# Performance work log

Measured on AMD Instinct MI355X. Metric: run time of the kernel, lower is better.

## Reference

```python
import jax, jax.numpy as jnp
import numpy as np

N_NODES = 50000
N_EDGES = 640000
D = 128      # in_feats
OUT = 128    # out_feats


def setup_inputs() -> dict:
    key = jax.random.key(0)
    ks = jax.random.split(key, 8)
    feat = jax.random.normal(ks[0], (N_NODES, D), dtype=jnp.float32)
    weight = jax.random.uniform(ks[1], (N_EDGES,), dtype=jnp.float32)
    src = jax.random.randint(ks[2], (N_EDGES,), 0, N_NODES, dtype=jnp.int64)
    dst = jax.random.randint(ks[3], (N_EDGES,), 0, N_NODES, dtype=jnp.int64)
    # xavier_uniform with relu gain ~ sqrt(2)*sqrt(6/(fan_in+fan_out))
    g = np.sqrt(2.0)
    lim_pool = g * np.sqrt(6.0 / (D + D))
    lim_neigh = g * np.sqrt(6.0 / (2 * D + OUT))
    W_pool = jax.random.uniform(ks[4], (D, D), dtype=jnp.float32, minval=-lim_pool, maxval=lim_pool)
    b_pool = jnp.zeros((D,), dtype=jnp.float32)
    W_neigh = jax.random.uniform(ks[5], (OUT, 2 * D), dtype=jnp.float32, minval=-lim_neigh, maxval=lim_neigh)
    b_neigh = jnp.zeros((OUT,), dtype=jnp.float32)
    return {"feat": feat, "weight": weight, "src": src, "dst": dst,
            "W_pool": W_pool, "b_pool": b_pool, "W_neigh": W_neigh, "b_neigh": b_neigh}


def reference(feat, weight, src, dst, W_pool, b_pool, W_neigh, b_neigh):
    n = feat.shape[0]
    # fc_pool: h = feat @ W_pool.T + b_pool  -> [N, D]
    h = feat @ W_pool.T + b_pool
    # u_mul_e: per-edge message m_e = h[src_e] * w_e  -> [E, D]
    m = h[src] * weight[:, None]
    # max reduce over incoming edges (scatter-max by dst)
    neigh = jax.ops.segment_max(m, dst, num_segments=n)
    # zero-degree nodes get 0 (segment_max fills empties with -inf)
    deg = jax.ops.segment_sum(jnp.ones_like(weight), dst, num_segments=n)
    neigh = jnp.where(deg[:, None] > 0, neigh, jnp.zeros((), dtype=feat.dtype))
    # fc_neigh on concat(feat, neigh)
    rst = jnp.concatenate([feat, neigh], axis=1) @ W_neigh.T + b_neigh
    return rst
```

## Files before the change

kernel.cpp:

```cpp
#include <hip/hip_runtime.h>
#include <cstdint>
#include <cstddef>

#define N_NODES 50000
#define N_EDGES 640000
#define DF 128

#define NBUCK 196
#define BCAP  6144
#define PA_BLOCKS 250

typedef __attribute__((ext_vector_type(8))) short bf16x8;
typedef __attribute__((ext_vector_type(4))) float f32x4;

__device__ inline unsigned short f2bf(float f) {
    unsigned int u = __float_as_uint(f);
    return (unsigned short)((u + 0x7fffu + ((u >> 16) & 1u)) >> 16);
}

#define NF4 (N_NODES * DF / 4)
#define NWG (3 * 2048)
__global__ __launch_bounds__(256) void k1_setup_bucket(
    const float* __restrict__ feat,
    const float* __restrict__ W_pool,
    const float* __restrict__ W_neigh,
    const int* __restrict__ src,
    const int* __restrict__ dst,
    const float* __restrict__ w,
    unsigned short* __restrict__ featb,
    unsigned short* __restrict__ Wp_f,
    unsigned short* __restrict__ Wn1_f,
    unsigned short* __restrict__ Wn2_f,
    int* __restrict__ bucketcnt,
    uint2* __restrict__ staging)
{
    int bid = blockIdx.x;
    int t = threadIdx.x;
    if (bid < PA_BLOCKS) {
        __shared__ int cnt[NBUCK];
        __shared__ int runbase[NBUCK];
        int base = bid * 2560;
        if (t < NBUCK) cnt[t] = 0;
        __syncthreads();
        uint2 rec[10];
        int bk[10];
        #pragma unroll
        for (int i = 0; i < 10; ++i) {
            int e = base + i * 256 + t;
            int s = src[e], d = dst[e];
            bk[i] = d >> 8;
            rec[i].x = (unsigned int)s | ((unsigned int)(d & 255) << 16);
            rec[i].y = __float_as_uint(w[e]);
            atomicAdd(&cnt[bk[i]], 1);
        }
        __syncthreads();
        if (t < NBUCK) {
            runbase[t] = atomicAdd(&bucketcnt[t], cnt[t]);
            cnt[t] = 0;
        }
        __syncthreads();
        #pragma unroll
        for (int i = 0; i < 10; ++i) {
            int r = atomicAdd(&cnt[bk[i]], 1);
            int pos = runbase[bk[i]] + r;
            if (pos < BCAP) staging[bk[i] * BCAP + pos] = rec[i];
        }
    } else if (bid < 250 + NF4 / 256) {
        int idx = (bid - PA_BLOCKS) * 256 + t;
        float4 v = ((const float4*)feat)[idx];
        ushort4 o;
        o.x = f2bf(v.x); o.y = f2bf(v.y); o.z = f2bf(v.z); o.w = f2bf(v.w);
        ((ushort4*)featb)[idx] = o;
    } else {
        int g = (bid - PA_BLOCKS - NF4 / 256) * 256 + t;
        int m = g >> 11;
        int r8 = g & 2047;
        int L = r8 & 63, tt = (r8 >> 6) & 3, c = r8 >> 8;
        int o = c * 16 + (L & 15);
        int kb = tt * 32 + (L >> 4) * 8;
        const float* srcp;
        unsigned short* dstp;
        if (m == 0)      { srcp = W_pool  + o * 128 + kb;       dstp = Wp_f;  }
        else if (m == 1) { srcp = W_neigh + o * 256 + kb;       dstp = Wn1_f; }
        else             { srcp = W_neigh + o * 256 + 128 + kb; dstp = Wn2_f; }
        ushort4 lo, hi;
        float4 a = ((const float4*)srcp)[0];
        float4 b = ((const float4*)srcp)[1];
        lo.x = f2bf(a.x); lo.y = f2bf(a.y); lo.z = f2bf(a.z); lo.w = f2bf(a.w);
        hi.x = f2bf(b.x); hi.y = f2bf(b.y); hi.z = f2bf(b.z); hi.w = f2bf(b.w);
        ((ushort4*)(dstp + r8 * 8))[0] = lo;
        ((ushort4*)(dstp + r8 * 8))[1] = hi;
    }
}

#define GEMMB 196
__global__ __launch_bounds__(1024) void k2_gemm_passb(
    const unsigned short* __restrict__ featb,
    const unsigned short* __restrict__ Wp_f,
    const float* __restrict__ b_pool,
    unsigned short* __restrict__ hb,
    const int* __restrict__ bucketcnt,
    const uint2* __restrict__ staging,
    int* __restrict__ offsets,
    uint2* __restrict__ edges)
{
    int t = threadIdx.x;
    if (blockIdx.x < GEMMB) {
        int wave = blockIdx.x * 16 + (t >> 6);
        int lane = t & 63;
        int m0 = wave * 16;
        if (m0 >= N_NODES) return;
        const int n = lane & 15, quad = lane >> 4;

        f32x4 acc[8];
        #pragma unroll
        for (int c = 0; c < 8; ++c) {
            float bv = b_pool[c * 16 + n];
            acc[c] = (f32x4){bv, bv, bv, bv};
        }
        const unsigned short* aptr = featb + (size_t)(m0 + n) * DF + quad * 8;
        #pragma unroll
        for (int tt = 0; tt < 4; ++tt) {
            bf16x8 af = *(const bf16x8*)(aptr + tt * 32);
            #pragma unroll
            for (int c = 0; c < 8; ++c) {
                bf16x8 bf = *(const bf16x8*)(Wp_f + (size_t)((c * 4 + tt) * 64 + lane) * 8);
                acc[c] = __builtin_amdgcn_mfma_f32_16x16x32_bf16(af, bf, acc[c], 0, 0, 0);
            }
        }
        #pragma unroll
        for (int c = 0; c < 8; ++c)
            #pragma unroll
            for (int r = 0; r < 4; ++r)
                hb[(size_t)(m0 + quad * 4 + r) * DF + c * 16 + n] = f2bf(acc[c][r]);
    } else {
        __shared__ int dcnt[256];
        __shared__ int sc[256];
        __shared__ int bc[256];
        int b = blockIdx.x - GEMMB;

        if (t < 256) { dcnt[t] = 0; bc[t] = (t < NBUCK) ? bucketcnt[t] : 0; sc[t] = (t < NBUCK) ? bc[t] : 0; }
        __syncthreads();
        #pragma unroll
        for (int off = 1; off < 256; off <<= 1) {
            int u = (t < 256 && t >= off) ? sc[t - off] : 0;
            __syncthreads();
            if (t < 256) sc[t] += u;
            __syncthreads();
        }
        int mybase = (b > 0) ? sc[b - 1] : 0;
        int cnt = bc[b];
        __syncthreads();

        uint2 rec[6];
        int nit = (cnt + 1023) >> 10;
        for (int i = 0; i < nit; ++i) {
            int idx = i * 1024 + t;
            if (idx < cnt) {
                rec[i] = staging[(size_t)b * BCAP + idx];
                atomicAdd(&dcnt[(rec[i].x >> 16) & 255], 1);
            }
        }
        __syncthreads();
        if (t < 256) sc[t] = dcnt[t];
        __syncthreads();
        #pragma unroll
        for (int off = 1; off < 256; off <<= 1) {
            int u = (t < 256 && t >= off) ? sc[t - off] : 0;
            __syncthreads();
            if (t < 256) sc[t] += u;
            __syncthreads();
        }
        if (t < 256) {
            int node = b * 256 + t;
            int excl = sc[t] - dcnt[t];
            if (node < N_NODES) offsets[node] = mybase + excl;
            dcnt[t] = mybase + excl;
        }
        if (b == NBUCK - 1 && t == 0) offsets[N_NODES] = mybase + cnt;
        __syncthreads();
        for (int i = 0; i < nit; ++i) {
            int idx = i * 1024 + t;
            if (idx < cnt) {
                int dl = (rec[i].x >> 16) & 255;
                int pos = atomicAdd(&dcnt[dl], 1);
                uint2 fin;
                fin.x = rec[i].x & 0xFFFFu;
                fin.y = rec[i].y;
                edges[pos] = fin;
            }
        }
    }
}

__global__ __launch_bounds__(256) void neigh_max_kernel(
    const unsigned short* __restrict__ hb, const int* __restrict__ offsets,
    const uint2* __restrict__ edges,
    unsigned short* __restrict__ neighb)
{
    int gwave = (blockIdx.x * 256 + threadIdx.x) >> 6;
    if (gwave >= N_NODES) return;
    int node = __builtin_amdgcn_readfirstlane(gwave);
    int lane = threadIdx.x & 63;
    const int half = lane >> 5;
    const int q = lane & 31;

    int beg = offsets[node], end = offsets[node + 1];
    float4 acc = make_float4(-3.4e38f, -3.4e38f, -3.4e38f, -3.4e38f);

    for (int e = beg; e < end; e += 8) {
        int i1 = min(e + 1, end - 1);
        int i2 = min(e + 2, end - 1);
        int i3 = min(e + 3, end - 1);
        int i4 = min(e + 4, end - 1);
        int i5 = min(e + 5, end - 1);
        int i6 = min(e + 6, end - 1);
        int i7 = min(e + 7, end - 1);
        uint2 e0 = edges[e],  e1 = edges[i1], e2 = edges[i2], e3 = edges[i3];
        uint2 e4 = edges[i4], e5 = edges[i5], e6 = edges[i6], e7 = edges[i7];
        uint2 mA = half ? e1 : e0;
        uint2 mB = half ? e3 : e2;
        uint2 mC = half ? e5 : e4;
        uint2 mD = half ? e7 : e6;
        float wA = __uint_as_float(mA.y);
        float wB = __uint_as_float(mB.y);
        float wC = __uint_as_float(mC.y);
        float wD = __uint_as_float(mD.y);
        uint2 pA = *(const uint2*)(hb + (size_t)mA.x * DF + q * 4);
        uint2 pB = *(const uint2*)(hb + (size_t)mB.x * DF + q * 4);
        uint2 pC = *(const uint2*)(hb + (size_t)mC.x * DF + q * 4);
        uint2 pD = *(const uint2*)(hb + (size_t)mD.x * DF + q * 4);
        acc.x = fmaxf(acc.x, __uint_as_float(pA.x << 16)          * wA);
        acc.y = fmaxf(acc.y, __uint_as_float(pA.x & 0xffff0000u)  * wA);
        acc.z = fmaxf(acc.z, __uint_as_float(pA.y << 16)          * wA);
        acc.w = fmaxf(acc.w, __uint_as_float(pA.y & 0xffff0000u)  * wA);
        acc.x = fmaxf(acc.x, __uint_as_float(pB.x << 16)          * wB);
        acc.y = fmaxf(acc.y, __uint_as_float(pB.x & 0xffff0000u)  * wB);
        acc.z = fmaxf(acc.z, __uint_as_float(pB.y << 16)          * wB);
        acc.w = fmaxf(acc.w, __uint_as_float(pB.y & 0xffff0000u)  * wB);
        acc.x = fmaxf(acc.x, __uint_as_float(pC.x << 16)          * wC);
        acc.y = fmaxf(acc.y, __uint_as_float(pC.x & 0xffff0000u)  * wC);
        acc.z = fmaxf(acc.z, __uint_as_float(pC.y << 16)          * wC);
        acc.w = fmaxf(acc.w, __uint_as_float(pC.y & 0xffff0000u)  * wC);
        acc.x = fmaxf(acc.x, __uint_as_float(pD.x << 16)          * wD);
        acc.y = fmaxf(acc.y, __uint_as_float(pD.x & 0xffff0000u)  * wD);
        acc.z = fmaxf(acc.z, __uint_as_float(pD.y << 16)          * wD);
        acc.w = fmaxf(acc.w, __uint_as_float(pD.y & 0xffff0000u)  * wD);
    }

    float4 o;
    o.x = fmaxf(acc.x, __shfl_xor(acc.x, 32));
    o.y = fmaxf(acc.y, __shfl_xor(acc.y, 32));
    o.z = fmaxf(acc.z, __shfl_xor(acc.z, 32));
    o.w = fmaxf(acc.w, __shfl_xor(acc.w, 32));
    if (beg == end) o = make_float4(0.f, 0.f, 0.f, 0.f);
    if (half == 0) {
        ushort4 ob;
        ob.x = f2bf(o.x); ob.y = f2bf(o.y); ob.z = f2bf(o.z); ob.w = f2bf(o.w);
        *(ushort4*)(neighb + (size_t)node * DF + q * 4) = ob;
    }
}

__global__ __launch_bounds__(256) void gemm_out(
    const unsigned short* __restrict__ featb,
    const unsigned short* __restrict__ neighb,
    const unsigned short* __restrict__ Wn1_f,
    const unsigned short* __restrict__ Wn2_f,
    const float* __restrict__ bias,
    float* __restrict__ out)
{
    int wave = (blockIdx.x * 256 + threadIdx.x) >> 6;
    int lane = threadIdx.x & 63;
    int m0 = wave * 16;
    if (m0 >= N_NODES) return;
    const int n = lane & 15, quad = lane >> 4;

    f32x4 acc[8];
    #pragma unroll
    for (int c = 0; c < 8; ++c) {
        float bv = bias[c * 16 + n];
        acc[c] = (f32x4){bv, bv, bv, bv};
    }

    const unsigned short* a0 = featb  + (size_t)(m0 + n) * DF + quad * 8;
    const unsigned short* a1 = neighb + (size_t)(m0 + n) * DF + quad * 8;
    #pragma unroll
    for (int t = 0; t < 4; ++t) {
        bf16x8 af = *(const bf16x8*)(a0 + t * 32);
        #pragma unroll
        for (int c = 0; c < 8; ++c) {
            bf16x8 bf = *(const bf16x8*)(Wn1_f + (size_t)((c * 4 + t) * 64 + lane) * 8);
            acc[c] = __builtin_amdgcn_mfma_f32_16x16x32_bf16(af, bf, acc[c], 0, 0, 0);
        }
    }
    #pragma unroll
    for (int t = 0; t < 4; ++t) {
        bf16x8 af = *(const bf16x8*)(a1 + t * 32);
        #pragma unroll
        for (int c = 0; c < 8; ++c) {
            bf16x8 bf = *(const bf16x8*)(Wn2_f + (size_t)((c * 4 + t) * 64 + lane) * 8);
            acc[c] = __builtin_amdgcn_mfma_f32_16x16x32_bf16(af, bf, acc[c], 0, 0, 0);
        }
    }

    #pragma unroll
    for (int c = 0; c < 8; ++c)
        #pragma unroll
        for (int r = 0; r < 4; ++r)
            out[(size_t)(m0 + quad * 4 + r) * DF + c * 16 + n] = acc[c][r];
}

extern "C" void kernel_launch(void* const* d_in, const int* in_sizes, int n_in,
                              void* d_out, int out_size, void* d_ws, size_t ws_size,
                              hipStream_t stream) {
    const float* feat    = (const float*)d_in[0];
    const float* weight  = (const float*)d_in[1];
    const int*   src     = (const int*)d_in[2];
    const int*   dst     = (const int*)d_in[3];
    const float* W_pool  = (const float*)d_in[4];
    const float* b_pool  = (const float*)d_in[5];
    const float* W_neigh = (const float*)d_in[6];
    const float* b_neigh = (const float*)d_in[7];
    float* out = (float*)d_out;

    char* ws = (char*)d_ws;
    unsigned short* featb  = (unsigned short*)(ws);
    unsigned short* hb     = (unsigned short*)(ws + 12800000);
    unsigned short* neighb = (unsigned short*)(ws + 25600000);
    unsigned short* Wp_f   = (unsigned short*)(ws + 38400000);
    unsigned short* Wn1_f  = (unsigned short*)(ws + 38432768);
    unsigned short* Wn2_f  = (unsigned short*)(ws + 38465536);
    int*   offsets   = (int*)  (ws + 38498304);
    int*   bucketcnt = (int*)  (ws + 38698368);
    uint2* staging   = (uint2*)(ws + 38699392);
    uint2* edges     = (uint2*)(ws + 48333184);

    hipMemsetAsync(bucketcnt, 0, 1024, stream);

    const int K1_BLOCKS = PA_BLOCKS + NF4 / 256 + NWG / 256;
    k1_setup_bucket<<<K1_BLOCKS, 256, 0, stream>>>(
        feat, W_pool, W_neigh, src, dst, weight,
        featb, Wp_f, Wn1_f, Wn2_f, bucketcnt, staging);

    k2_gemm_passb<<<GEMMB + NBUCK, 1024, 0, stream>>>(
        featb, Wp_f, b_pool, hb, bucketcnt, staging, offsets, edges);

    neigh_max_kernel<<<(N_NODES + 3) / 4, 256, 0, stream>>>(hb, offsets, edges, neighb);

    gemm_out<<<782, 256, 0, stream>>>(
        featb, neighb, Wn1_f, Wn2_f, b_neigh, out);
}
```

Baseline: 163.1 us.

## Fuse neighbor max aggregation with output GEMM via shared-memory tile

Merges the segment-max gather kernel and the output MFMA GEMM into one kernel. Each 256-thread block reduces 16 destination nodes into an LDS tile, then its four waves each compute two 16-column output chunks from that tile plus featb. This removes the neighb round-trip through global memory and one kernel launch. In exchange, each wave processes four nodes serially, and the block barrier makes waves wait on the highest-degree node in the tile, which may reduce latency hiding in the gather.

```diff
diff --git a/kernel.cpp b/kernel.cpp
--- a/kernel.cpp
+++ b/kernel.cpp
@@ -9,6 +9,7 @@
 #define NBUCK 196
 #define BCAP  6144
 #define PA_BLOCKS 250
+#define LPAD 136
 
 typedef __attribute__((ext_vector_type(8))) short bf16x8;
 typedef __attribute__((ext_vector_type(4))) float f32x4;
@@ -193,121 +194,116 @@
     }
 }
 
-__global__ __launch_bounds__(256) void neigh_max_kernel(
-    const unsigned short* __restrict__ hb, const int* __restrict__ offsets,
+__global__ __launch_bounds__(256) void neigh_out(
+    const unsigned short* __restrict__ featb,
+    const unsigned short* __restrict__ hb,
+    const int* __restrict__ offsets,
     const uint2* __restrict__ edges,
-    unsigned short* __restrict__ neighb)
-{
-    int gwave = (blockIdx.x * 256 + threadIdx.x) >> 6;
-    if (gwave >= N_NODES) return;
-    int node = __builtin_amdgcn_readfirstlane(gwave);
-    int lane = threadIdx.x & 63;
-    const int half = lane >> 5;
-    const int q = lane & 31;
-
-    int beg = offsets[node], end = offsets[node + 1];
-    float4 acc = make_float4(-3.4e38f, -3.4e38f, -3.4e38f, -3.4e38f);
-
-    for (int e = beg; e < end; e += 8) {
-        int i1 = min(e + 1, end - 1);
-        int i2 = min(e + 2, end - 1);
-        int i3 = min(e + 3, end - 1);
-        int i4 = min(e + 4, end - 1);
-        int i5 = min(e + 5, end - 1);
-        int i6 = min(e + 6, end - 1);
-        int i7 = min(e + 7, end - 1);
-        uint2 e0 = edges[e],  e1 = edges[i1], e2 = edges[i2], e3 = edges[i3];
-        uint2 e4 = edges[i4], e5 = edges[i5], e6 = edges[i6], e7 = edges[i7];
-        uint2 mA = half ? e1 : e0;
-        uint2 mB = half ? e3 : e2;
-        uint2 mC = half ? e5 : e4;
-        uint2 mD = half ? e7 : e6;
-        float wA = __uint_as_float(mA.y);
-        float wB = __uint_as_float(mB.y);
-        float wC = __uint_as_float(mC.y);
-        float wD = __uint_as_float(mD.y);
-        uint2 pA = *(const uint2*)(hb + (size_t)mA.x * DF + q * 4);
-        uint2 pB = *(const uint2*)(hb + (size_t)mB.x * DF + q * 4);
-        uint2 pC = *(const uint2*)(hb + (size_t)mC.x * DF + q * 4);
-        uint2 pD = *(const uint2*)(hb + (size_t)mD.x * DF + q * 4);
-        acc.x = fmaxf(acc.x, __uint_as_float(pA.x << 16)          * wA);
-        acc.y = fmaxf(acc.y, __uint_as_float(pA.x & 0xffff0000u)  * wA);
-        acc.z = fmaxf(acc.z, __uint_as_float(pA.y << 16)          * wA);
-        acc.w = fmaxf(acc.w, __uint_as_float(pA.y & 0xffff0000u)  * wA);
-        acc.x = fmaxf(acc.x, __uint_as_float(pB.x << 16)          * wB);
-        acc.y = fmaxf(acc.y, __uint_as_float(pB.x & 0xffff0000u)  * wB);
-        acc.z = fmaxf(acc.z, __uint_as_float(pB.y << 16)          * wB);
-        acc.w = fmaxf(acc.w, __uint_as_float(pB.y & 0xffff0000u)  * wB);
-        acc.x = fmaxf(acc.x, __uint_as_float(pC.x << 16)          * wC);
-        acc.y = fmaxf(acc.y, __uint_as_float(pC.x & 0xffff0000u)  * wC);
-        acc.z = fmaxf(acc.z, __uint_as_float(pC.y << 16)          * wC);
-        acc.w = fmaxf(acc.w, __uint_as_float(pC.y & 0xffff0000u)  * wC);
-        acc.x = fmaxf(acc.x, __uint_as_float(pD.x << 16)          * wD);
-        acc.y = fmaxf(acc.y, __uint_as_float(pD.x & 0xffff0000u)  * wD);
-        acc.z = fmaxf(acc.z, __uint_as_float(pD.y << 16)          * wD);
-        acc.w = fmaxf(acc.w, __uint_as_float(pD.y & 0xffff0000u)  * wD);
-    }
-
-    float4 o;
-    o.x = fmaxf(acc.x, __shfl_xor(acc.x, 32));
-    o.y = fmaxf(acc.y, __shfl_xor(acc.y, 32));
-    o.z = fmaxf(acc.z, __shfl_xor(acc.z, 32));
-    o.w = fmaxf(acc.w, __shfl_xor(acc.w, 32));
-    if (beg == end) o = make_float4(0.f, 0.f, 0.f, 0.f);
-    if (half == 0) {
-        ushort4 ob;
-        ob.x = f2bf(o.x); ob.y = f2bf(o.y); ob.z = f2bf(o.z); ob.w = f2bf(o.w);
-        *(ushort4*)(neighb + (size_t)node * DF + q * 4) = ob;
-    }
-}
-
-__global__ __launch_bounds__(256) void gemm_out(
-    const unsigned short* __restrict__ featb,
-    const unsigned short* __restrict__ neighb,
     const unsigned short* __restrict__ Wn1_f,
     const unsigned short* __restrict__ Wn2_f,
     const float* __restrict__ bias,
     float* __restrict__ out)
 {
-    int wave = (blockIdx.x * 256 + threadIdx.x) >> 6;
-    int lane = threadIdx.x & 63;
-    int m0 = wave * 16;
-    if (m0 >= N_NODES) return;
+    __shared__ unsigned short nl[16 * LPAD];
+    const int t = threadIdx.x;
+    const int wv = t >> 6;
+    const int lane = t & 63;
+    const int m0 = blockIdx.x * 16;
+    const int half = lane >> 5;
+    const int q = lane & 31;
+
+    for (int i = 0; i < 4; ++i) {
+        int node = m0 + wv * 4 + i;
+        int beg = offsets[node], end = offsets[node + 1];
+        float4 acc = make_float4(-3.4e38f, -3.4e38f, -3.4e38f, -3.4e38f);
+        for (int e = beg; e < end; e += 8) {
+            int i1 = min(e + 1, end - 1);
+            int i2 = min(e + 2, end - 1);
+            int i3 = min(e + 3, end - 1);
+            int i4 = min(e + 4, end - 1);
+            int i5 = min(e + 5, end - 1);
+            int i6 = min(e + 6, end - 1);
+            int i7 = min(e + 7, end - 1);
+            uint2 e0 = edges[e],  e1 = edges[i1], e2 = edges[i2], e3 = edges[i3];
+            uint2 e4 = edges[i4], e5 = edges[i5], e6 = edges[i6], e7 = edges[i7];
+            uint2 mA = half ? e1 : e0;
+            uint2 mB = half ? e3 : e2;
+            uint2 mC = half ? e5 : e4;
+            uint2 mD = half ? e7 : e6;
+            float wA = __uint_as_float(mA.y);
+            float wB = __uint_as_float(mB.y);
+            float wC = __uint_as_float(mC.y);
+            float wD = __uint_as_float(mD.y);
+            uint2 pA = *(const uint2*)(hb + (size_t)mA.x * DF + q * 4);
+            uint2 pB = *(const uint2*)(hb + (size_t)mB.x * DF + q * 4);
+            uint2 pC = *(const uint2*)(hb + (size_t)mC.x * DF + q * 4);
+            uint2 pD = *(const uint2*)(hb + (size_t)mD.x * DF + q * 4);
+            acc.x = fmaxf(acc.x, __uint_as_float(pA.x << 16)          * wA);
+            acc.y = fmaxf(acc.y, __uint_as_float(pA.x & 0xffff0000u)  * wA);
+            acc.z = fmaxf(acc.z, __uint_as_float(pA.y << 16)          * wA);
+            acc.w = fmaxf(acc.w, __uint_as_float(pA.y & 0xffff0000u)  * wA);
+            acc.x = fmaxf(acc.x, __uint_as_float(pB.x << 16)          * wB);
+            acc.y = fmaxf(acc.y, __uint_as_float(pB.x & 0xffff0000u)  * wB);
+            acc.z = fmaxf(acc.z, __uint_as_float(pB.y << 16)          * wB);
+            acc.w = fmaxf(acc.w, __uint_as_float(pB.y & 0xffff0000u)  * wB);
+            acc.x = fmaxf(acc.x, __uint_as_float(pC.x << 16)          * wC);
+            acc.y = fmaxf(acc.y, __uint_as_float(pC.x & 0xffff0000u)  * wC);
+            acc.z = fmaxf(acc.z, __uint_as_float(pC.y << 16)          * wC);
+            acc.w = fmaxf(acc.w, __uint_as_float(pC.y & 0xffff0000u)  * wC);
+            acc.x = fmaxf(acc.x, __uint_as_float(pD.x << 16)          * wD);
+            acc.y = fmaxf(acc.y, __uint_as_float(pD.x & 0xffff0000u)  * wD);
+            acc.z = fmaxf(acc.z, __uint_as_float(pD.y << 16)          * wD);
+            acc.w = fmaxf(acc.w, __uint_as_float(pD.y & 0xffff0000u)  * wD);
+        }
+        float4 o;
+        o.x = fmaxf(acc.x, __shfl_xor(acc.x, 32));
+        o.y = fmaxf(acc.y, __shfl_xor(acc.y, 32));
+        o.z = fmaxf(acc.z, __shfl_xor(acc.z, 32));
+        o.w = fmaxf(acc.w, __shfl_xor(acc.w, 32));
+        if (beg == end) o = make_float4(0.f, 0.f, 0.f, 0.f);
+        if (half == 0) {
+            ushort4 ob;
+            ob.x = f2bf(o.x); ob.y = f2bf(o.y); ob.z = f2bf(o.z); ob.w = f2bf(o.w);
+            *(ushort4*)(&nl[(wv * 4 + i) * LPAD + q * 4]) = ob;
+        }
+    }
+    __syncthreads();
+
     const int n = lane & 15, quad = lane >> 4;
-
-    f32x4 acc[8];
+    f32x4 acc[2];
     #pragma unroll
-    for (int c = 0; c < 8; ++c) {
-        float bv = bias[c * 16 + n];
-        acc[c] = (f32x4){bv, bv, bv, bv};
-    }
-
-    const unsigned short* a0 = featb  + (size_t)(m0 + n) * DF + quad * 8;
-    const unsigned short* a1 = neighb + (size_t)(m0 + n) * DF + quad * 8;
+    for (int cc = 0; cc < 2; ++cc) {
+        float bv = bias[(wv * 2 + cc) * 16 + n];
+        acc[cc] = (f32x4){bv, bv, bv, bv};
+    }
+
+    const unsigned short* a0 = featb + (size_t)(m0 + n) * DF + quad * 8;
     #pragma unroll
-    for (int t = 0; t < 4; ++t) {
-        bf16x8 af = *(const bf16x8*)(a0 + t * 32);
-        #pragma unroll
-        for (int c = 0; c < 8; ++c) {
-            bf16x8 bf = *(const bf16x8*)(Wn1_f + (size_t)((c * 4 + t) * 64 + lane) * 8);
-            acc[c] = __builtin_amdgcn_mfma_f32_16x16x32_bf16(af, bf, acc[c], 0, 0, 0);
+    for (int tt = 0; tt < 4; ++tt) {
+        bf16x8 af = *(const bf16x8*)(a0 + tt * 32);
+        #pragma unroll
+        for (int cc = 0; cc < 2; ++cc) {
+            int c = wv * 2 + cc;
+            bf16x8 bf = *(const bf16x8*)(Wn1_f + (size_t)((c * 4 + tt) * 64 + lane) * 8);
+            acc[cc] = __builtin_amdgcn_mfma_f32_16x16x32_bf16(af, bf, acc[cc], 0, 0, 0);
         }
     }
     #pragma unroll
-    for (int t = 0; t < 4; ++t) {
-        bf16x8 af = *(const bf16x8*)(a1 + t * 32);
-        #pragma unroll
-        for (int c = 0; c < 8; ++c) {
-            bf16x8 bf = *(const bf16x8*)(Wn2_f + (size_t)((c * 4 + t) * 64 + lane) * 8);
-            acc[c] = __builtin_amdgcn_mfma_f32_16x16x32_bf16(af, bf, acc[c], 0, 0, 0);
+    for (int tt = 0; tt < 4; ++tt) {
+        bf16x8 af = *(const bf16x8*)(&nl[n * LPAD + tt * 32 + quad * 8]);
+        #pragma unroll
+        for (int cc = 0; cc < 2; ++cc) {
+            int c = wv * 2 + cc;
+            bf16x8 bf = *(const bf16x8*)(Wn2_f + (size_t)((c * 4 + tt) * 64 + lane) * 8);
+            acc[cc] = __builtin_amdgcn_mfma_f32_16x16x32_bf16(af, bf, acc[cc], 0, 0, 0);
         }
     }
 
     #pragma unroll
-    for (int c = 0; c < 8; ++c)
+    for (int cc = 0; cc < 2; ++cc)
         #pragma unroll
         for (int r = 0; r < 4; ++r)
-            out[(size_t)(m0 + quad * 4 + r) * DF + c * 16 + n] = acc[c][r];
+            out[(size_t)(m0 + quad * 4 + r) * DF + (wv * 2 + cc) * 16 + n] = acc[cc][r];
 }
 
 extern "C" void kernel_launch(void* const* d_in, const int* in_sizes, int n_in,
@@ -326,14 +322,13 @@
     char* ws = (char*)d_ws;
     unsigned short* featb  = (unsigned short*)(ws);
     unsigned short* hb     = (unsigned short*)(ws + 12800000);
-    unsigned short* neighb = (unsigned short*)(ws + 25600000);
-    unsigned short* Wp_f   = (unsigned short*)(ws + 38400000);
-    unsigned short* Wn1_f  = (unsigned short*)(ws + 38432768);
-    unsigned short* Wn2_f  = (unsigned short*)(ws + 38465536);
-    int*   offsets   = (int*)  (ws + 38498304);
-    int*   bucketcnt = (int*)  (ws + 38698368);
-    uint2* staging   = (uint2*)(ws + 38699392);
-    uint2* edges     = (uint2*)(ws + 48333184);
+    unsigned short* Wp_f   = (unsigned short*)(ws + 25600000);
+    unsigned short* Wn1_f  = (unsigned short*)(ws + 25632768);
+    unsigned short* Wn2_f  = (unsigned short*)(ws + 25665536);
+    int*   offsets   = (int*)  (ws + 25698304);
+    int*   bucketcnt = (int*)  (ws + 25898368);
+    uint2* staging   = (uint2*)(ws + 25899392);
+    uint2* edges     = (uint2*)(ws + 35533184);
 
     hipMemsetAsync(bucketcnt, 0, 1024, stream);
 
@@ -345,8 +340,6 @@
     k2_gemm_passb<<<GEMMB + NBUCK, 1024, 0, stream>>>(
         featb, Wp_f, b_pool, hb, bucketcnt, staging, offsets, edges);
 
-    neigh_max_kernel<<<(N_NODES + 3) / 4, 256, 0, stream>>>(hb, offsets, edges, neighb);
-
-    gemm_out<<<782, 256, 0, stream>>>(
-        featb, neighb, Wn1_f, Wn2_f, b_neigh, out);
-}
+    neigh_out<<<N_NODES / 16, 256, 0, stream>>>(
+        featb, hb, offsets, edges, Wn1_f, Wn2_f, b_neigh, out);
+}
```

Result: slower. 177.9 us (+9.1%).
